# Kernel tuning notes

Hardware: AMD Instinct MI355X
Metric: run time of the kernel (lower is better)

## Reference

```python
import jax, jax.numpy as jnp
import numpy as np

B, S, D = 2, 4096, 1024
H = 4096           # hidden_dim = 4*dim
E = 8              # expert_count
K = 4              # expert_capacity (top-k)


def setup_inputs() -> dict:
    key = jax.random.key(0)
    kx, kr, ku, kd = jax.random.split(key, 4)
    x = jax.random.normal(kx, (B, S, D), dtype=jnp.float32)
    # Dense kernels (flax stores as [in, out]); lecun-normal-ish scaling
    router_w = jax.random.normal(kr, (D, E), dtype=jnp.float32) / np.sqrt(D)
    up_w = jax.random.normal(ku, (E, D, H), dtype=jnp.float32) / np.sqrt(D)
    down_w = jax.random.normal(kd, (E, H, D), dtype=jnp.float32) / np.sqrt(H)
    return {"x": x, "router_w": router_w, "up_w": up_w, "down_w": down_w}


def reference(x, router_w, up_w, down_w):
    # Router: softmax over experts, then top-k selection (expert_capacity)
    router_logits = jnp.einsum('bsd,de->bse', x, router_w)          # [B,S,E]
    routing_weights = jax.nn.softmax(router_logits, axis=-1)
    topk_weights, topk_indices = jax.lax.top_k(routing_weights, K)  # [B,S,K]
    topk_weights = topk_weights / jnp.sum(topk_weights, axis=-1, keepdims=True)

    # Dense all-expert MLP (as in the original module): [B,S,E,D]
    h = jnp.einsum('bsd,edh->bseh', x, up_w)                        # [B,S,E,H]
    h = jax.nn.gelu(h)                                              # tanh-approx, flax default
    expert_outputs = jnp.einsum('bseh,ehd->bsed', h, down_w)        # [B,S,E,D]

    # Gather selected experts and combine with normalized weights
    gathered = jnp.take_along_axis(expert_outputs,
                                   topk_indices[:, :, :, None], axis=2)  # [B,S,K,D]
    output = jnp.sum(topk_weights[:, :, :, None] * gathered, axis=2)     # [B,S,D]
    return output
```

## Files before the change

kernel.cpp:

```cpp
#include <hip/hip_runtime.h>
#include <stdint.h>

typedef unsigned short u16;
typedef unsigned int u32;
typedef __attribute__((ext_vector_type(8))) short bf16x8;
typedef __attribute__((ext_vector_type(4))) float f32x4;

#define NTOK 8192
#define DDIM 1024
#define HDIM 4096
#define NEXP 8
#define KSEL 4
#define TILE 128
#define BK 32
#define SLOTCAP 33792
#define MAXMT (SLOTCAP / TILE)

__device__ __forceinline__ u16 f2bf(float f) {
  union { float f; u32 u; } v; v.f = f;
  u32 r = v.u + 0x7fffu + ((v.u >> 16) & 1u);
  return (u16)(r >> 16);
}

__device__ __forceinline__ void gl_lds16(const void* g, void* l) {
  __builtin_amdgcn_global_load_lds(
      (__attribute__((address_space(1))) u32*)(uintptr_t)g,
      (__attribute__((address_space(3))) u32*)l, 16, 0, 0);
}

__device__ __forceinline__ float gelu_t(float x) {
  float u = 0.7978845608028654f * (x + 0.044715f * x * x * x);
  float e = __expf(2.0f * u);
  float th = 1.0f - 2.0f / (e + 1.0f);
  return 0.5f * x * (1.0f + th);
}

__global__ void k_cvt_x(const float* __restrict__ x, u16* __restrict__ xb) {
  int i = blockIdx.x * blockDim.x + threadIdx.x;
  float4 v = ((const float4*)x)[i];
  uint2 p;
  p.x = (u32)f2bf(v.x) | ((u32)f2bf(v.y) << 16);
  p.y = (u32)f2bf(v.z) | ((u32)f2bf(v.w) << 16);
  ((uint2*)xb)[i] = p;
}

__global__ void k_transpose_bf16(const float* __restrict__ in, u16* __restrict__ out,
                                 int R, int C) {
  __shared__ float tile[32][33];
  int e = blockIdx.z;
  const float* src = in + (size_t)e * R * C;
  u16* dst = out + (size_t)e * R * C;
  int c0 = blockIdx.x * 32, r0 = blockIdx.y * 32;
  int tx = threadIdx.x, ty = threadIdx.y;
#pragma unroll
  for (int i = 0; i < 4; i++)
    tile[ty + i * 8][tx] = src[(size_t)(r0 + ty + i * 8) * C + c0 + tx];
  __syncthreads();
#pragma unroll
  for (int i = 0; i < 4; i++)
    dst[(size_t)(c0 + ty + i * 8) * R + r0 + tx] = f2bf(tile[tx][ty + i * 8]);
}

__global__ void k_topk(const float* __restrict__ x, const float* __restrict__ rw,
                       int* __restrict__ eid, float* __restrict__ tw) {
  int token = blockIdx.x * 4 + (threadIdx.x >> 6);
  int lane = threadIdx.x & 63;
  const float* xr = x + (size_t)token * DDIM;
  float p[NEXP];
#pragma unroll
  for (int e = 0; e < NEXP; e++) p[e] = 0.f;
  for (int it = 0; it < DDIM / 64; ++it) {
    int j = it * 64 + lane;
    float xj = xr[j];
    const float* r = rw + (size_t)j * NEXP;
    float4 a = *(const float4*)r;
    float4 b = *(const float4*)(r + 4);
    p[0] += xj * a.x; p[1] += xj * a.y; p[2] += xj * a.z; p[3] += xj * a.w;
    p[4] += xj * b.x; p[5] += xj * b.y; p[6] += xj * b.z; p[7] += xj * b.w;
  }
#pragma unroll
  for (int off = 32; off; off >>= 1) {
#pragma unroll
    for (int e = 0; e < NEXP; e++) p[e] += __shfl_xor(p[e], off);
  }
  unsigned used = 0;
  int idx[KSEL]; float lg[KSEL];
#pragma unroll
  for (int k = 0; k < KSEL; k++) {
    float bv = -1e30f; int bi = 0;
#pragma unroll
    for (int e = 0; e < NEXP; e++)
      if (!((used >> e) & 1) && p[e] > bv) { bv = p[e]; bi = e; }
    used |= 1u << bi; idx[k] = bi; lg[k] = bv;
  }
  float wv[KSEL]; float wsum = 0.f;
#pragma unroll
  for (int k = 0; k < KSEL; k++) { wv[k] = __expf(lg[k] - lg[0]); wsum += wv[k]; }
  float inv = 1.f / wsum;
  if (lane < KSEL) {
    eid[token * KSEL + lane] = idx[lane];
    tw[token * KSEL + lane] = wv[lane] * inv;
  }
}

__global__ void k_offsets(const int* __restrict__ eid, int* __restrict__ poff) {
  __shared__ int cnt[NEXP];
  if (threadIdx.x < NEXP) cnt[threadIdx.x] = 0;
  __syncthreads();
  int l0=0,l1=0,l2=0,l3=0,l4=0,l5=0,l6=0,l7=0;
  for (int i = threadIdx.x; i < NTOK * KSEL; i += 256) {
    int v = eid[i];
    l0 += (v == 0); l1 += (v == 1); l2 += (v == 2); l3 += (v == 3);
    l4 += (v == 4); l5 += (v == 5); l6 += (v == 6); l7 += (v == 7);
  }
  atomicAdd(&cnt[0], l0); atomicAdd(&cnt[1], l1);
  atomicAdd(&cnt[2], l2); atomicAdd(&cnt[3], l3);
  atomicAdd(&cnt[4], l4); atomicAdd(&cnt[5], l5);
  atomicAdd(&cnt[6], l6); atomicAdd(&cnt[7], l7);
  __syncthreads();
  if (threadIdx.x == 0) {
    int acc = 0;
#pragma unroll
    for (int e = 0; e < NEXP; e++) {
      poff[e] = acc;
      acc += ((cnt[e] + TILE - 1) / TILE) * TILE;
    }
    poff[NEXP] = acc;
  }
}

__global__ void k_scatter(const int* __restrict__ eid, const float* __restrict__ tw,
                          const int* __restrict__ poff,
                          int* __restrict__ tok_cmb, float* __restrict__ w_cmb) {
  int e = blockIdx.x;
  int base = poff[e];
  __shared__ int wave_tot[16];
  __shared__ int running;
  if (threadIdx.x == 0) running = 0;
  __syncthreads();
  int lane = threadIdx.x & 63, wave = threadIdx.x >> 6;
  for (int c = 0; c < NTOK * KSEL; c += 1024) {
    int i = c + threadIdx.x;
    bool f = (eid[i] == e);
    unsigned long long m = __ballot(f);
    int wexcl = __popcll(m & ((1ull << lane) - 1ull));
    if (lane == 0) wave_tot[wave] = __popcll(m);
    __syncthreads();
    int rbase = running;
    int wbase = 0;
    for (int wv = 0; wv < wave; wv++) wbase += wave_tot[wv];
    if (f) {
      int pos = base + rbase + wbase + wexcl;
      tok_cmb[pos] = i >> 2;
      w_cmb[pos] = tw[i];
    }
    __syncthreads();
    if (threadIdx.x == 0) {
      int s = 0;
#pragma unroll
      for (int wv = 0; wv < 16; wv++) s += wave_tot[wv];
      running = rbase + s;
    }
    __syncthreads();
  }
}

template <bool IS_UP>
__global__ __launch_bounds__(256) void k_moe_gemm(
    const u16* __restrict__ A, const u16* __restrict__ Bbase,
    const int* __restrict__ tok_cmb, const float* __restrict__ w_cmb,
    const int* __restrict__ poff,
    u16* __restrict__ act, float* __restrict__ out, int e_fixed) {
  const int mtile = blockIdx.y;
  const int pbase = (e_fixed >= 0) ? poff[e_fixed] : 0;
  const int pend = (e_fixed >= 0) ? poff[e_fixed + 1] : poff[NEXP];
  const int slot0 = pbase + mtile * TILE;
  if (slot0 >= pend) return;
  int e;
  if (e_fixed >= 0) {
    e = e_fixed;
  } else {
    e = 0;
#pragma unroll
    for (int i = 1; i < NEXP; i++) e += (slot0 >= poff[i]);
  }
  const int ntile = blockIdx.x;
  const int K = IS_UP ? DDIM : HDIM;
  const u16* B = Bbase + (size_t)e * HDIM * DDIM;

  __shared__ u16 As[TILE * BK];
  __shared__ u16 Bs[TILE * BK];

  const int t = threadIdx.x, lane = t & 63, wave = t >> 6;
  const int ar = t >> 2, akb = (t & 3) * 8;
  int row0, row1;
  if (IS_UP) {
    row0 = tok_cmb[slot0 + ar];
    row1 = tok_cmb[slot0 + ar + 64];
  } else {
    row0 = mtile * TILE + ar;
    row1 = row0 + 64;
  }
  const u16* gA0 = A + (size_t)row0 * K + akb;
  const u16* gA1 = A + (size_t)row1 * K + akb;
  const int bn = ntile * TILE + ar;
  const u16* gB0 = B + (size_t)bn * K + akb;
  const u16* gB1 = gB0 + (size_t)64 * K;

  u16* AsW = As + wave * 512;
  u16* BsW = Bs + wave * 512;

  f32x4 acc[4][4];
#pragma unroll
  for (int m = 0; m < 4; m++)
#pragma unroll
    for (int n = 0; n < 4; n++) acc[m][n] = (f32x4){0.f, 0.f, 0.f, 0.f};

  const int wm = wave >> 1, wn = wave & 1;
  const int fr = lane & 15, fk = (lane >> 4) * 8;

  for (int k0 = 0; k0 < K; k0 += BK) {
    gl_lds16(gA0 + k0, AsW);
    gl_lds16(gA1 + k0, AsW + 2048);
    gl_lds16(gB0 + k0, BsW);
    gl_lds16(gB1 + k0, BsW + 2048);
    __syncthreads();
    bf16x8 a[4], b[4];
#pragma unroll
    for (int m = 0; m < 4; m++) a[m] = *(const bf16x8*)&As[(wm * 64 + m * 16 + fr) * BK + fk];
#pragma unroll
    for (int n = 0; n < 4; n++) b[n] = *(const bf16x8*)&Bs[(wn * 64 + n * 16 + fr) * BK + fk];
#pragma unroll
    for (int m = 0; m < 4; m++)
#pragma unroll
      for (int n = 0; n < 4; n++)
        acc[m][n] = __builtin_amdgcn_mfma_f32_16x16x32_bf16(a[m], b[n], acc[m][n], 0, 0, 0);
    __syncthreads();
  }

  if (IS_UP) {
#pragma unroll
    for (int m = 0; m < 4; m++) {
#pragma unroll
      for (int j = 0; j < 4; j++) {
        int r = wm * 64 + m * 16 + (lane >> 4) * 4 + j;
        size_t rowoff = (size_t)(mtile * TILE + r) * HDIM + (size_t)ntile * TILE;
#pragma unroll
        for (int n = 0; n < 4; n++) {
          int c = wn * 64 + n * 16 + fr;
          act[rowoff + c] = f2bf(gelu_t(acc[m][n][j]));
        }
      }
    }
  } else {
#pragma unroll
    for (int m = 0; m < 4; m++) {
#pragma unroll
      for (int j = 0; j < 4; j++) {
        int r = wm * 64 + m * 16 + (lane >> 4) * 4 + j;
        int slot = slot0 + r;
        int tok = tok_cmb[slot];
        float w = w_cmb[slot];
        float* orow = out + (size_t)tok * DDIM + (size_t)ntile * TILE;
#pragma unroll
        for (int n = 0; n < 4; n++) {
          int c = wn * 64 + n * 16 + fr;
          atomicAdd(&orow[c], w * acc[m][n][j]);
        }
      }
    }
  }
}

extern "C" void kernel_launch(void* const* d_in, const int* in_sizes, int n_in,
                              void* d_out, int out_size, void* d_ws, size_t ws_size,
                              hipStream_t stream) {
  const float* x  = (const float*)d_in[0];
  const float* rw = (const float*)d_in[1];
  const float* up = (const float*)d_in[2];
  const float* dw = (const float*)d_in[3];
  float* out = (float*)d_out;

  char* ws = (char*)d_ws;
  size_t off = 0;
  u16* xb = (u16*)(ws + off);      off += (size_t)NTOK * DDIM * 2;
  u16* upbT = (u16*)(ws + off);    off += (size_t)NEXP * HDIM * DDIM * 2;
  u16* downbT = (u16*)(ws + off);  off += (size_t)NEXP * DDIM * HDIM * 2;
  int* eid = (int*)(ws + off);     off += (size_t)NTOK * KSEL * 4;
  float* tw = (float*)(ws + off);  off += (size_t)NTOK * KSEL * 4;
  int* poff = (int*)(ws + off);    off += 64;
  int* tok_cmb = (int*)(ws + off); off += (size_t)SLOTCAP * 4;
  float* w_cmb = (float*)(ws + off); off += (size_t)SLOTCAP * 4;
  u16* act = (u16*)(ws + off);
  size_t need_big = off + (size_t)SLOTCAP * HDIM * 2;
  const bool big = (ws_size >= need_big);

  hipMemsetAsync(d_out, 0, (size_t)NTOK * DDIM * 4, stream);
  hipMemsetAsync(tok_cmb, 0, (size_t)SLOTCAP * 8, stream);

  k_cvt_x<<<dim3(NTOK * DDIM / 4 / 256), dim3(256), 0, stream>>>(x, xb);
  k_transpose_bf16<<<dim3(HDIM / 32, DDIM / 32, NEXP), dim3(32, 8), 0, stream>>>(up, upbT, DDIM, HDIM);
  k_transpose_bf16<<<dim3(DDIM / 32, HDIM / 32, NEXP), dim3(32, 8), 0, stream>>>(dw, downbT, HDIM, DDIM);
  k_topk<<<dim3(NTOK / 4), dim3(256), 0, stream>>>(x, rw, eid, tw);
  k_offsets<<<dim3(1), dim3(256), 0, stream>>>(eid, poff);
  k_scatter<<<dim3(NEXP), dim3(1024), 0, stream>>>(eid, tw, poff, tok_cmb, w_cmb);

  if (big) {
    k_moe_gemm<true><<<dim3(HDIM / TILE, MAXMT), dim3(256), 0, stream>>>(
        xb, upbT, tok_cmb, w_cmb, poff, act, out, -1);
    k_moe_gemm<false><<<dim3(DDIM / TILE, MAXMT), dim3(256), 0, stream>>>(
        act, downbT, tok_cmb, w_cmb, poff, act, out, -1);
  } else {
    for (int e = 0; e < NEXP; e++) {
      k_moe_gemm<true><<<dim3(HDIM / TILE, NTOK / TILE), dim3(256), 0, stream>>>(
          xb, upbT, tok_cmb, w_cmb, poff, act, out, e);
      k_moe_gemm<false><<<dim3(DDIM / TILE, NTOK / TILE), dim3(256), 0, stream>>>(
          act, downbT, tok_cmb, w_cmb, poff, act, out, e);
    }
  }
}
```

Measured before the change: 1.079 ms.

## Rewrite MoE grouped GEMM with 256x256 tiles, 4-stage LDS pipeline, XCD remap

Replaces the single-buffered 128x128 grouped GEMM with a 256x256 tile using 8 waves, a four-deep LDS ring fed by async global-to-LDS loads, and explicit waitcnt and barrier scheduling. This overlaps memory traffic with MFMA work. It also adds an XOR swizzle to cut LDS bank conflicts and remaps workgroups across XCDs for L2 locality. Expert padding grows to 256 rows, so more padded slots get computed, and the larger tile raises register and LDS pressure.

Measured after the change: 1.295 ms. +20.0%, slower.

```diff
diff --git a/kernel.cpp b/kernel.cpp
--- a/kernel.cpp
+++ b/kernel.cpp
@@ -11,10 +11,10 @@
 #define HDIM 4096
 #define NEXP 8
 #define KSEL 4
-#define TILE 128
+#define BM 256
 #define BK 32
-#define SLOTCAP 33792
-#define MAXMT (SLOTCAP / TILE)
+#define SLOTCAP 35072
+#define MAXMT (SLOTCAP / BM)
 
 __device__ __forceinline__ u16 f2bf(float f) {
   union { float f; u32 u; } v; v.f = f;
@@ -123,7 +123,7 @@
 #pragma unroll
     for (int e = 0; e < NEXP; e++) {
       poff[e] = acc;
-      acc += ((cnt[e] + TILE - 1) / TILE) * TILE;
+      acc += ((cnt[e] + BM - 1) / BM) * BM;
     }
     poff[NEXP] = acc;
   }
@@ -165,16 +165,76 @@
   }
 }
 
+template <int ST, int VM>
+__device__ __forceinline__ void tile_body(
+    int T, char* ldsA, char* ldsB,
+    bf16x8 (&afr)[8], bf16x8 (&bfr)[4], f32x4 (&acc)[8][4],
+    const int (&aoff)[8], const int (&boff)[4],
+    const char*& aS0, const char*& aS1, const char*& bS0, const char*& bS1,
+    int w1024) {
+  const char* Ab = ldsA + (T & 3) * 16384;
+  const char* Bb = ldsB + (T & 3) * 16384;
+  char* AbS = ldsA + ((T + 3) & 3) * 16384;
+  char* BbS = ldsB + ((T + 3) & 3) * 16384;
+#pragma unroll
+  for (int mb = 0; mb < 4; ++mb) afr[mb] = *(const bf16x8*)(Ab + aoff[mb]);
+#pragma unroll
+  for (int nb = 0; nb < 4; ++nb) bfr[nb] = *(const bf16x8*)(Bb + boff[nb]);
+  if (ST) { gl_lds16(aS0, AbS + w1024); gl_lds16(aS1, AbS + 8192 + w1024); }
+  __builtin_amdgcn_s_barrier();
+  asm volatile("s_waitcnt lgkmcnt(0)" ::: "memory");
+  __builtin_amdgcn_sched_barrier(0);
+  __builtin_amdgcn_s_setprio(1);
+#pragma unroll
+  for (int mb = 0; mb < 4; ++mb)
+#pragma unroll
+    for (int nb = 0; nb < 4; ++nb)
+      acc[mb][nb] = __builtin_amdgcn_mfma_f32_16x16x32_bf16(afr[mb], bfr[nb], acc[mb][nb], 0, 0, 0);
+  __builtin_amdgcn_s_setprio(0);
+  __builtin_amdgcn_s_barrier();
+  __builtin_amdgcn_sched_barrier(0);
+#pragma unroll
+  for (int mb = 4; mb < 8; ++mb) afr[mb] = *(const bf16x8*)(Ab + aoff[mb]);
+  if (ST) {
+    gl_lds16(bS0, BbS + w1024); gl_lds16(bS1, BbS + 8192 + w1024);
+    aS0 += 64; aS1 += 64; bS0 += 64; bS1 += 64;
+  }
+  if (VM == 8) asm volatile("s_waitcnt vmcnt(8)" ::: "memory");
+  else if (VM == 4) asm volatile("s_waitcnt vmcnt(4)" ::: "memory");
+  else if (VM == 0) asm volatile("s_waitcnt vmcnt(0)" ::: "memory");
+  __builtin_amdgcn_sched_barrier(0);
+  __builtin_amdgcn_s_barrier();
+  asm volatile("s_waitcnt lgkmcnt(0)" ::: "memory");
+  __builtin_amdgcn_sched_barrier(0);
+  __builtin_amdgcn_s_setprio(1);
+#pragma unroll
+  for (int mb = 4; mb < 8; ++mb)
+#pragma unroll
+    for (int nb = 0; nb < 4; ++nb)
+      acc[mb][nb] = __builtin_amdgcn_mfma_f32_16x16x32_bf16(afr[mb], bfr[nb], acc[mb][nb], 0, 0, 0);
+  __builtin_amdgcn_s_setprio(0);
+  __builtin_amdgcn_s_barrier();
+  __builtin_amdgcn_sched_barrier(0);
+}
+
 template <bool IS_UP>
-__global__ __launch_bounds__(256) void k_moe_gemm(
+__global__ __launch_bounds__(512, 2) void k_moe_gemm(
     const u16* __restrict__ A, const u16* __restrict__ Bbase,
     const int* __restrict__ tok_cmb, const float* __restrict__ w_cmb,
     const int* __restrict__ poff,
     u16* __restrict__ act, float* __restrict__ out, int e_fixed) {
-  const int mtile = blockIdx.y;
+  int nx = gridDim.x;
+  int nwg = nx * gridDim.y;
+  int flat = blockIdx.y * nx + blockIdx.x;
+  int q = nwg >> 3, r = nwg & 7;
+  int xcd = flat & 7, sub = flat >> 3;
+  int wgid = (xcd < r ? xcd * (q + 1) : r * (q + 1) + (xcd - r) * q) + sub;
+  int ntile = wgid % nx;
+  int mtile = wgid / nx;
+
   const int pbase = (e_fixed >= 0) ? poff[e_fixed] : 0;
   const int pend = (e_fixed >= 0) ? poff[e_fixed + 1] : poff[NEXP];
-  const int slot0 = pbase + mtile * TILE;
+  const int slot0 = pbase + mtile * BM;
   if (slot0 >= pend) return;
   int e;
   if (e_fixed >= 0) {
@@ -184,89 +244,99 @@
 #pragma unroll
     for (int i = 1; i < NEXP; i++) e += (slot0 >= poff[i]);
   }
-  const int ntile = blockIdx.x;
   const int K = IS_UP ? DDIM : HDIM;
+  const int NT = K / BK;
+  const size_t ROWB = (size_t)K * 2;
   const u16* B = Bbase + (size_t)e * HDIM * DDIM;
 
-  __shared__ u16 As[TILE * BK];
-  __shared__ u16 Bs[TILE * BK];
-
-  const int t = threadIdx.x, lane = t & 63, wave = t >> 6;
-  const int ar = t >> 2, akb = (t & 3) * 8;
-  int row0, row1;
+  __shared__ u16 AsBuf[4 * 8192];
+  __shared__ u16 BsBuf[4 * 8192];
+  char* ldsA = (char*)AsBuf;
+  char* ldsB = (char*)BsBuf;
+
+  const int t = threadIdx.x, lane = t & 63, w = t >> 6;
+  const int w1024 = w << 10;
+  const int wm = w >> 2, wn = w & 3;
+  const int fr = lane & 15, fkb = (lane >> 4) * 16;
+
+  const int srow0 = w * 16 + (lane >> 2);
+  const int srow1 = 128 + srow0;
+  const int kb = ((lane & 3) * 16) ^ (((lane >> 5) & 1) << 5);
+  size_t aRow0, aRow1;
   if (IS_UP) {
-    row0 = tok_cmb[slot0 + ar];
-    row1 = tok_cmb[slot0 + ar + 64];
+    aRow0 = (size_t)tok_cmb[slot0 + srow0] * ROWB;
+    aRow1 = (size_t)tok_cmb[slot0 + srow1] * ROWB;
   } else {
-    row0 = mtile * TILE + ar;
-    row1 = row0 + 64;
-  }
-  const u16* gA0 = A + (size_t)row0 * K + akb;
-  const u16* gA1 = A + (size_t)row1 * K + akb;
-  const int bn = ntile * TILE + ar;
-  const u16* gB0 = B + (size_t)bn * K + akb;
-  const u16* gB1 = gB0 + (size_t)64 * K;
-
-  u16* AsW = As + wave * 512;
-  u16* BsW = Bs + wave * 512;
-
-  f32x4 acc[4][4];
-#pragma unroll
-  for (int m = 0; m < 4; m++)
-#pragma unroll
-    for (int n = 0; n < 4; n++) acc[m][n] = (f32x4){0.f, 0.f, 0.f, 0.f};
-
-  const int wm = wave >> 1, wn = wave & 1;
-  const int fr = lane & 15, fk = (lane >> 4) * 8;
-
-  for (int k0 = 0; k0 < K; k0 += BK) {
-    gl_lds16(gA0 + k0, AsW);
-    gl_lds16(gA1 + k0, AsW + 2048);
-    gl_lds16(gB0 + k0, BsW);
-    gl_lds16(gB1 + k0, BsW + 2048);
-    __syncthreads();
-    bf16x8 a[4], b[4];
-#pragma unroll
-    for (int m = 0; m < 4; m++) a[m] = *(const bf16x8*)&As[(wm * 64 + m * 16 + fr) * BK + fk];
-#pragma unroll
-    for (int n = 0; n < 4; n++) b[n] = *(const bf16x8*)&Bs[(wn * 64 + n * 16 + fr) * BK + fk];
-#pragma unroll
-    for (int m = 0; m < 4; m++)
-#pragma unroll
-      for (int n = 0; n < 4; n++)
-        acc[m][n] = __builtin_amdgcn_mfma_f32_16x16x32_bf16(a[m], b[n], acc[m][n], 0, 0, 0);
-    __syncthreads();
-  }
+    aRow0 = (size_t)(mtile * BM + srow0) * ROWB;
+    aRow1 = (size_t)(mtile * BM + srow1) * ROWB;
+  }
+  const char* aS0 = (const char*)A + aRow0 + kb;
+  const char* aS1 = (const char*)A + aRow1 + kb;
+  const char* bS0 = (const char*)B + (size_t)(ntile * BM + srow0) * ROWB + kb;
+  const char* bS1 = (const char*)B + (size_t)(ntile * BM + srow1) * ROWB + kb;
+
+  int aoff[8], boff[4];
+#pragma unroll
+  for (int mb = 0; mb < 8; ++mb) {
+    int row = wm * 128 + mb * 16 + fr;
+    aoff[mb] = (row * 64 + fkb) ^ ((((row >> 3) & 1)) << 5);
+  }
+#pragma unroll
+  for (int nb = 0; nb < 4; ++nb) {
+    int row = wn * 64 + nb * 16 + fr;
+    boff[nb] = (row * 64 + fkb) ^ ((((row >> 3) & 1)) << 5);
+  }
+
+  f32x4 acc[8][4];
+#pragma unroll
+  for (int mb = 0; mb < 8; ++mb)
+#pragma unroll
+    for (int nb = 0; nb < 4; ++nb) acc[mb][nb] = (f32x4){0.f, 0.f, 0.f, 0.f};
+  bf16x8 afr[8], bfr[4];
+
+#pragma unroll
+  for (int tt = 0; tt < 3; ++tt) {
+    char* AbS = ldsA + tt * 16384;
+    char* BbS = ldsB + tt * 16384;
+    gl_lds16(aS0, AbS + w1024); gl_lds16(aS1, AbS + 8192 + w1024);
+    gl_lds16(bS0, BbS + w1024); gl_lds16(bS1, BbS + 8192 + w1024);
+    aS0 += 64; aS1 += 64; bS0 += 64; bS1 += 64;
+  }
+  asm volatile("s_waitcnt vmcnt(8)" ::: "memory");
+  __builtin_amdgcn_sched_barrier(0);
+  __builtin_amdgcn_s_barrier();
+
+  for (int T = 0; T < NT - 3; ++T)
+    tile_body<1, 8>(T, ldsA, ldsB, afr, bfr, acc, aoff, boff, aS0, aS1, bS0, bS1, w1024);
+  tile_body<0, 4>(NT - 3, ldsA, ldsB, afr, bfr, acc, aoff, boff, aS0, aS1, bS0, bS1, w1024);
+  tile_body<0, 0>(NT - 2, ldsA, ldsB, afr, bfr, acc, aoff, boff, aS0, aS1, bS0, bS1, w1024);
+  tile_body<0, -1>(NT - 1, ldsA, ldsB, afr, bfr, acc, aoff, boff, aS0, aS1, bS0, bS1, w1024);
 
   if (IS_UP) {
 #pragma unroll
-    for (int m = 0; m < 4; m++) {
-#pragma unroll
-      for (int j = 0; j < 4; j++) {
-        int r = wm * 64 + m * 16 + (lane >> 4) * 4 + j;
-        size_t rowoff = (size_t)(mtile * TILE + r) * HDIM + (size_t)ntile * TILE;
-#pragma unroll
-        for (int n = 0; n < 4; n++) {
-          int c = wn * 64 + n * 16 + fr;
-          act[rowoff + c] = f2bf(gelu_t(acc[m][n][j]));
-        }
+    for (int mb = 0; mb < 8; ++mb) {
+#pragma unroll
+      for (int jj = 0; jj < 4; ++jj) {
+        int rr = mtile * BM + wm * 128 + mb * 16 + (lane >> 4) * 4 + jj;
+        u16* arow = act + (size_t)rr * HDIM + (size_t)ntile * BM + wn * 64;
+#pragma unroll
+        for (int nb = 0; nb < 4; ++nb)
+          arow[nb * 16 + fr] = f2bf(gelu_t(acc[mb][nb][jj]));
       }
     }
   } else {
 #pragma unroll
-    for (int m = 0; m < 4; m++) {
-#pragma unroll
-      for (int j = 0; j < 4; j++) {
-        int r = wm * 64 + m * 16 + (lane >> 4) * 4 + j;
-        int slot = slot0 + r;
+    for (int mb = 0; mb < 8; ++mb) {
+#pragma unroll
+      for (int jj = 0; jj < 4; ++jj) {
+        int rloc = wm * 128 + mb * 16 + (lane >> 4) * 4 + jj;
+        int slot = slot0 + rloc;
         int tok = tok_cmb[slot];
-        float w = w_cmb[slot];
-        float* orow = out + (size_t)tok * DDIM + (size_t)ntile * TILE;
-#pragma unroll
-        for (int n = 0; n < 4; n++) {
-          int c = wn * 64 + n * 16 + fr;
-          atomicAdd(&orow[c], w * acc[m][n][j]);
-        }
+        float wgt = w_cmb[slot];
+        float* orow = out + (size_t)tok * DDIM + (size_t)ntile * BM + wn * 64;
+#pragma unroll
+        for (int nb = 0; nb < 4; ++nb)
+          atomicAdd(&orow[nb * 16 + fr], wgt * acc[mb][nb][jj]);
       }
     }
   }
@@ -306,15 +376,15 @@
   k_scatter<<<dim3(NEXP), dim3(1024), 0, stream>>>(eid, tw, poff, tok_cmb, w_cmb);
 
   if (big) {
-    k_moe_gemm<true><<<dim3(HDIM / TILE, MAXMT), dim3(256), 0, stream>>>(
+    k_moe_gemm<true><<<dim3(HDIM / BM, MAXMT), dim3(512), 0, stream>>>(
         xb, upbT, tok_cmb, w_cmb, poff, act, out, -1);
-    k_moe_gemm<false><<<dim3(DDIM / TILE, MAXMT), dim3(256), 0, stream>>>(
+    k_moe_gemm<false><<<dim3(DDIM / BM, MAXMT), dim3(512), 0, stream>>>(
         act, downbT, tok_cmb, w_cmb, poff, act, out, -1);
   } else {
     for (int e = 0; e < NEXP; e++) {
-      k_moe_gemm<true><<<dim3(HDIM / TILE, NTOK / TILE), dim3(256), 0, stream>>>(
+      k_moe_gemm<true><<<dim3(HDIM / BM, NTOK / BM), dim3(512), 0, stream>>>(
           xb, upbT, tok_cmb, w_cmb, poff, act, out, e);
-      k_moe_gemm<false><<<dim3(DDIM / TILE, NTOK / TILE), dim3(256), 0, stream>>>(
+      k_moe_gemm<false><<<dim3(DDIM / BM, NTOK / BM), dim3(512), 0, stream>>>(
           act, downbT, tok_cmb, w_cmb, poff, act, out, e);
     }
   }
```
